# Kernel optimization log

Measured on AMD Instinct MI355X. Metric: run time of the kernel, lower is better.

## Reference

```python
import jax, jax.numpy as jnp
import numpy as np
from jax import lax

WS = 8        # window size
NH = 4        # num heads
HD = 32       # head dim
DIM = NH * HD # 128
SCALE = HD ** -0.5


def _rel_index(ws):
    coords = np.stack(np.meshgrid(np.arange(ws), np.arange(ws), indexing='ij'))  # (2,ws,ws)
    cf = coords.reshape(2, -1)                      # (2, N)
    rel = cf[:, :, None] - cf[:, None, :]           # (2, N, N)
    rel = rel.transpose(1, 2, 0).astype(np.int64)   # (N, N, 2)
    rel[..., 0] += ws - 1
    rel[..., 1] += ws - 1
    rel[..., 0] *= 2 * ws - 1
    return jnp.asarray(rel.sum(-1))                 # (N, N)


def setup_inputs() -> dict:
    key = jax.random.key(0)
    ks = jax.random.split(key, 8)
    B, H, W = 8, 128, 128
    return {
        'x': jax.random.normal(ks[0], (B, DIM, H, W), jnp.float32),
        'qkv_w': jax.random.normal(ks[1], (DIM, 3 * DIM), jnp.float32) * 0.02,
        'qkv_b': jnp.zeros((3 * DIM,), jnp.float32),
        'proj_w': jax.random.normal(ks[2], (DIM, DIM), jnp.float32) * 0.02,
        'proj_b': jnp.zeros((DIM,), jnp.float32),
        'rpb_table': jax.random.normal(ks[3], ((2 * WS - 1) * (2 * WS - 1), NH), jnp.float32) * 0.02,
        'fc_w': jax.random.normal(ks[4], (9, 3 * NH), jnp.float32) * 0.1,   # 1x1 conv: (out=9, in=3*NH)
        'fc_b': jnp.zeros((9,), jnp.float32),
        'dep_w': jax.random.normal(ks[5], (DIM, 9, 3, 3), jnp.float32) * 0.1,  # grouped conv OIHW, groups=HD
        'dep_b': jnp.zeros((DIM,), jnp.float32),
        'rate1': jnp.array(0.5, jnp.float32),
        'rate2': jnp.array(0.5, jnp.float32),
    }


def reference(x, qkv_w, qkv_b, proj_w, proj_b, rpb_table, fc_w, fc_b, dep_w, dep_b, rate1, rate2):
    B, C, H, W = x.shape
    N = WS * WS
    xh = jnp.transpose(x, (0, 2, 3, 1))                 # (B,H,W,C)
    qkv = xh @ qkv_w + qkv_b                            # (B,H,W,3C)

    # ----- conv branch -----
    f_all = qkv.reshape(B, H * W, 3 * NH, HD).transpose(0, 2, 1, 3)       # (B,3NH,HW,HD)
    f_c = jnp.einsum('oc,bcnd->bond', fc_w, f_all) + fc_b[None, :, None, None]  # (B,9,HW,HD)
    f_conv = jnp.transpose(f_c, (0, 3, 1, 2)).reshape(B, HD * 9, H, W)    # (B,9*HD,H,W)
    out_conv = lax.conv_general_dilated(
        f_conv, dep_w, window_strides=(1, 1), padding=((1, 1), (1, 1)),
        dimension_numbers=('NCHW', 'OIHW', 'NCHW'), feature_group_count=HD)
    out_conv = jnp.transpose(out_conv + dep_b[None, :, None, None], (0, 2, 3, 1))  # (B,H,W,C)

    # ----- windowed attention branch -----
    nWh, nWw = H // WS, W // WS
    w = qkv.reshape(B, nWh, WS, nWw, WS, 3 * C).transpose(0, 1, 3, 2, 4, 5)
    w = w.reshape(B * nWh * nWw, N, 3, NH, HD).transpose(2, 0, 3, 1, 4)   # (3,Bw,NH,N,HD)
    q, k, v = w[0] * SCALE, w[1], w[2]
    attn = jnp.einsum('bhnd,bhmd->bhnm', q, k)                            # (Bw,NH,N,N)
    bias = rpb_table[_rel_index(WS)]                                      # (N,N,NH)
    attn = attn + jnp.transpose(bias, (2, 0, 1))[None]
    attn = jax.nn.softmax(attn, axis=-1)
    xa = jnp.einsum('bhnm,bhmd->bnhd', attn, v).reshape(-1, N, C)         # (Bw,N,C)
    xa = xa @ proj_w + proj_b
    xa = xa.reshape(B, nWh, nWw, WS, WS, C).transpose(0, 1, 3, 2, 4, 5).reshape(B, H, W, C)

    out = rate1 * xa + rate2 * out_conv
    return jnp.transpose(out, (0, 3, 1, 2))
```

## Files before the change

### kernel.cpp

```cpp
#include <hip/hip_runtime.h>

typedef unsigned short ushort_t;
typedef unsigned int uint_t;
typedef __attribute__((ext_vector_type(8))) short short8;
typedef __attribute__((ext_vector_type(4))) float f32x4;

#define SCALE 0.17677669529663687f

__device__ __forceinline__ float blo(uint_t u) { return __uint_as_float(u << 16); }
__device__ __forceinline__ float bhi(uint_t u) { return __uint_as_float(u & 0xffff0000u); }
__device__ __forceinline__ float u2f(ushort_t u) { return __uint_as_float(((uint_t)u) << 16); }
__device__ __forceinline__ ushort_t f2u(float f) {
    const uint_t x = __float_as_uint(f);
    return (ushort_t)((x + 0x7fffu + ((x >> 16) & 1u)) >> 16);
}
__device__ __forceinline__ uint_t pack2(float a, float b) {
    return (uint_t)f2u(a) | ((uint_t)f2u(b) << 16);
}

__device__ __forceinline__ float dot8(const float* qa, uint4 u) {
    return qa[0] * blo(u.x) + qa[1] * bhi(u.x) + qa[2] * blo(u.y) + qa[3] * bhi(u.y)
         + qa[4] * blo(u.z) + qa[5] * bhi(u.z) + qa[6] * blo(u.w) + qa[7] * bhi(u.w);
}
__device__ __forceinline__ void pv8(float* a, float e, uint4 u) {
    a[0] += e * blo(u.x); a[1] += e * bhi(u.x); a[2] += e * blo(u.y); a[3] += e * bhi(u.y);
    a[4] += e * blo(u.z); a[5] += e * bhi(u.z); a[6] += e * blo(u.w); a[7] += e * bhi(u.w);
}


__global__ __launch_bounds__(256) void k_qqkv(
    const float* __restrict__ x, const float* __restrict__ w,
    const float* __restrict__ wb, ushort_t* __restrict__ qkv)
{
    __shared__ ushort_t XT[128 * 128];
    __shared__ ushort_t WT[128 * 128];
    const int t = threadIdx.x;
    const int p0 = blockIdx.x * 128;
    const int b = p0 >> 14;
    const int rem = p0 & 16383;
    const float* xb = x + ((size_t)b << 21) + rem;

#pragma unroll
    for (int it = 0; it < 8; ++it) {
        const int slot = it * 256 + t;
        const int p = slot & 127, cb = slot >> 7;
        uint4 u;
        {
            const float a0 = xb[(size_t)(cb * 8 + 0) * 16384 + p];
            const float a1 = xb[(size_t)(cb * 8 + 1) * 16384 + p];
            const float a2 = xb[(size_t)(cb * 8 + 2) * 16384 + p];
            const float a3 = xb[(size_t)(cb * 8 + 3) * 16384 + p];
            const float a4 = xb[(size_t)(cb * 8 + 4) * 16384 + p];
            const float a5 = xb[(size_t)(cb * 8 + 5) * 16384 + p];
            const float a6 = xb[(size_t)(cb * 8 + 6) * 16384 + p];
            const float a7 = xb[(size_t)(cb * 8 + 7) * 16384 + p];
            u.x = pack2(a0, a1); u.y = pack2(a2, a3);
            u.z = pack2(a4, a5); u.w = pack2(a6, a7);
        }
        *(uint4*)&XT[p * 128 + ((cb ^ (p & 7)) << 3)] = u;
    }

    const int l = t & 63, wv = t >> 6;
    const int wj = (wv >> 1) * 64, wp = (wv & 1) * 64;
    const int lr = l & 15, lg = l >> 4;

    for (int jt = 0; jt < 3; ++jt) {
        const int j0 = jt * 128;
        __syncthreads();

#pragma unroll
        for (int it = 0; it < 8; ++it) {
            const int slot = it * 256 + t;
            const int j = slot & 127, cb = slot >> 7;
            uint4 u;
            {
                const float a0 = w[(size_t)(cb * 8 + 0) * 384 + j0 + j];
                const float a1 = w[(size_t)(cb * 8 + 1) * 384 + j0 + j];
                const float a2 = w[(size_t)(cb * 8 + 2) * 384 + j0 + j];
                const float a3 = w[(size_t)(cb * 8 + 3) * 384 + j0 + j];
                const float a4 = w[(size_t)(cb * 8 + 4) * 384 + j0 + j];
                const float a5 = w[(size_t)(cb * 8 + 5) * 384 + j0 + j];
                const float a6 = w[(size_t)(cb * 8 + 6) * 384 + j0 + j];
                const float a7 = w[(size_t)(cb * 8 + 7) * 384 + j0 + j];
                u.x = pack2(a0, a1); u.y = pack2(a2, a3);
                u.z = pack2(a4, a5); u.w = pack2(a6, a7);
            }
            *(uint4*)&WT[j * 128 + ((cb ^ (j & 7)) << 3)] = u;
        }
        __syncthreads();

        f32x4 acc[4][4];
#pragma unroll
        for (int i = 0; i < 4; ++i)
#pragma unroll
            for (int j = 0; j < 4; ++j) acc[i][j] = (f32x4){0.f, 0.f, 0.f, 0.f};

#pragma unroll
        for (int ks = 0; ks < 4; ++ks) {
            const int kb = ks * 4 + lg;
            short8 af[4], bf[4];
#pragma unroll
            for (int i = 0; i < 4; ++i) {
                const int jr = wj + i * 16 + lr;
                af[i] = *(const short8*)&WT[jr * 128 + ((kb ^ (jr & 7)) << 3)];
                const int pr = wp + i * 16 + lr;
                bf[i] = *(const short8*)&XT[pr * 128 + ((kb ^ (pr & 7)) << 3)];
            }
#pragma unroll
            for (int ji = 0; ji < 4; ++ji)
#pragma unroll
                for (int pi = 0; pi < 4; ++pi)
                    acc[ji][pi] = __builtin_amdgcn_mfma_f32_16x16x32_bf16(
                        af[ji], bf[pi], acc[ji][pi], 0, 0, 0);
        }
        __syncthreads();

#pragma unroll
        for (int ji = 0; ji < 4; ++ji) {
            const int jq = wj + ji * 16 + 4 * lg;
            const float4 bias = *(const float4*)&wb[j0 + jq];
#pragma unroll
            for (int pi = 0; pi < 4; ++pi) {
                const int p = wp + pi * 16 + lr;
                uint2 o;
                o.x = pack2(acc[ji][pi][0] + bias.x, acc[ji][pi][1] + bias.y);
                o.y = pack2(acc[ji][pi][2] + bias.z, acc[ji][pi][3] + bias.w);
                *(uint2*)&WT[p * 128 + (((jq >> 3) ^ (p & 7)) << 3) + (jq & 7)] = o;
            }
        }
        __syncthreads();

#pragma unroll
        for (int it = 0; it < 8; ++it) {
            const int slot = it * 256 + t;
            const int seg = slot & 15, p = slot >> 4;
            const uint4 v = *(const uint4*)&WT[p * 128 + ((seg ^ (p & 7)) << 3)];
            *(uint4*)&qkv[(size_t)(p0 + p) * 384 + j0 + seg * 8] = v;
        }
    }
}

__global__ __launch_bounds__(256) void k_attn4(
    const ushort_t* __restrict__ qkv, const float* __restrict__ rpb,
    float* __restrict__ out)
{
    __shared__ uint_t lds[13956];
    ushort_t* lds_sh = (ushort_t*)lds;
    float* rpbl = (float*)(lds + 13056);
    const int t = threadIdx.x;
    const int b = blockIdx.x >> 8, wy = (blockIdx.x >> 4) & 15, wx = blockIdx.x & 15;
    const int prow0 = (b << 14) + (wy * 8) * 128 + wx * 8;
    const uint_t* qkvu = (const uint_t*)qkv;

    for (int i = t; i < 4096; i += 256) {
        const int m = i >> 6, u = i & 63;
        const size_t pr = (size_t)(prow0 + (m >> 3) * 128 + (m & 7)) * 192;
        lds[m * 68 + u]        = qkvu[pr + u];
        lds[4352 + m * 68 + u] = qkvu[pr + 64 + u];
        const uint_t v = qkvu[pr + 128 + u];
        lds_sh[17408 + (2 * u) * 68 + m]     = (ushort_t)(v & 0xffffu);
        lds_sh[17408 + (2 * u + 1) * 68 + m] = (ushort_t)(v >> 16);
    }
    for (int i = t; i < 900; i += 256) rpbl[i] = rpb[i];
    __syncthreads();

    const int h = t >> 6, l = t & 63;
    const int lr = l & 15, lg = l >> 4;

    short8 af_k[4], bf_q[4];
#pragma unroll
    for (int i = 0; i < 4; ++i) {
        af_k[i] = *(const short8*)&lds_sh[8704 + (i * 16 + lr) * 136 + h * 32 + lg * 8];
        bf_q[i] = *(const short8*)&lds_sh[(i * 16 + lr) * 136 + h * 32 + lg * 8];
    }
    f32x4 sA[4][4];
#pragma unroll
    for (int nt = 0; nt < 4; ++nt)
#pragma unroll
        for (int mt = 0; mt < 4; ++mt)
            sA[nt][mt] = __builtin_amdgcn_mfma_f32_16x16x32_bf16(
                af_k[mt], bf_q[nt], (f32x4){0.f, 0.f, 0.f, 0.f}, 0, 0, 0);

    float inv[4];
#pragma unroll
    for (int nt = 0; nt < 4; ++nt) {
        const int n = nt * 16 + lr;
        const int ry = n >> 3, rx = n & 7;
        float mxv = -1e30f;
#pragma unroll
        for (int mt = 0; mt < 4; ++mt)
#pragma unroll
            for (int r = 0; r < 4; ++r) {
                const int m = mt * 16 + lg * 4 + r;
                const float bias =
                    rpbl[((ry - (m >> 3) + 7) * 15 + (rx - (m & 7) + 7)) * 4 + h];
                const float s = sA[nt][mt][r] * SCALE + bias;
                sA[nt][mt][r] = s;
                mxv = fmaxf(mxv, s);
            }
        mxv = fmaxf(mxv, __shfl_xor(mxv, 16));
        mxv = fmaxf(mxv, __shfl_xor(mxv, 32));
        float ls = 0.f;
#pragma unroll
        for (int mt = 0; mt < 4; ++mt)
#pragma unroll
            for (int r = 0; r < 4; ++r) {
                const float e = __expf(sA[nt][mt][r] - mxv);
                sA[nt][mt][r] = e;
                ls += e;
            }
        ls += __shfl_xor(ls, 16);
        ls += __shfl_xor(ls, 32);
        inv[nt] = 1.f / ls;
    }

    __syncthreads();

    uint_t* Pb = lds + h * 2176;
#pragma unroll
    for (int nt = 0; nt < 4; ++nt) {
        const int n = nt * 16 + lr;
#pragma unroll
        for (int mt = 0; mt < 4; ++mt) {
            uint2 o;
            o.x = pack2(sA[nt][mt][0], sA[nt][mt][1]);
            o.y = pack2(sA[nt][mt][2], sA[nt][mt][3]);
            *(uint2*)&Pb[n * 34 + mt * 8 + lg * 2] = o;
        }
    }
    asm volatile("s_waitcnt lgkmcnt(0)" ::: "memory");

    union U8 { short8 s8; uint2 u2[2]; };
    f32x4 oA[2][4];
#pragma unroll
    for (int dt = 0; dt < 2; ++dt)
#pragma unroll
        for (int nt = 0; nt < 4; ++nt) oA[dt][nt] = (f32x4){0.f, 0.f, 0.f, 0.f};
#pragma unroll
    for (int ks = 0; ks < 2; ++ks) {
        const int kb = ks * 4 + lg;
        short8 av[2], bp[4];
#pragma unroll
        for (int dt = 0; dt < 2; ++dt) {
            U8 u;
            const int d = h * 32 + dt * 16 + lr;
            u.u2[0] = *(const uint2*)&lds[8704 + d * 34 + kb * 4];
            u.u2[1] = *(const uint2*)&lds[8704 + d * 34 + kb * 4 + 2];
            av[dt] = u.s8;
        }
#pragma unroll
        for (int nt = 0; nt < 4; ++nt) {
            U8 u;
            const int n = nt * 16 + lr;
            u.u2[0] = *(const uint2*)&Pb[n * 34 + kb * 4];
            u.u2[1] = *(const uint2*)&Pb[n * 34 + kb * 4 + 2];
            bp[nt] = u.s8;
        }
#pragma unroll
        for (int dt = 0; dt < 2; ++dt)
#pragma unroll
            for (int nt = 0; nt < 4; ++nt)
                oA[dt][nt] = __builtin_amdgcn_mfma_f32_16x16x32_bf16(
                    av[dt], bp[nt], oA[dt][nt], 0, 0, 0);
    }

    float* ob = out + ((size_t)b << 21);
    const int pixbase = (wy * 8) * 128 + wx * 8;
#pragma unroll
    for (int dt = 0; dt < 2; ++dt)
#pragma unroll
        for (int nt = 0; nt < 4; ++nt) {
            const int n = nt * 16 + lr;
            const size_t po = (size_t)(pixbase + (n >> 3) * 128 + (n & 7));
            const float iv = inv[nt];
#pragma unroll
            for (int r = 0; r < 4; ++r) {
                const int d = h * 32 + dt * 16 + lg * 4 + r;
                ob[((size_t)d << 14) + po] = oA[dt][nt][r] * iv;
            }
        }
}

__global__ __launch_bounds__(256) void k_proj(
    const float* __restrict__ pw, const float* __restrict__ pb,
    const float* __restrict__ r1, float* __restrict__ out)
{
    __shared__ ushort_t XT[128 * 128];
    __shared__ ushort_t WT[128 * 128];
    const int t = threadIdx.x;
    const int p0 = blockIdx.x * 128;
    const int b = p0 >> 14;
    const int rem = p0 & 16383;
    const float* xb = out + ((size_t)b << 21) + rem;

#pragma unroll
    for (int it = 0; it < 8; ++it) {
        const int slot = it * 256 + t;
        const int p = slot & 127, cb = slot >> 7;
        uint4 u;
        {
            const float a0 = xb[(size_t)(cb * 8 + 0) * 16384 + p];
            const float a1 = xb[(size_t)(cb * 8 + 1) * 16384 + p];
            const float a2 = xb[(size_t)(cb * 8 + 2) * 16384 + p];
            const float a3 = xb[(size_t)(cb * 8 + 3) * 16384 + p];
            const float a4 = xb[(size_t)(cb * 8 + 4) * 16384 + p];
            const float a5 = xb[(size_t)(cb * 8 + 5) * 16384 + p];
            const float a6 = xb[(size_t)(cb * 8 + 6) * 16384 + p];
            const float a7 = xb[(size_t)(cb * 8 + 7) * 16384 + p];
            u.x = pack2(a0, a1); u.y = pack2(a2, a3);
            u.z = pack2(a4, a5); u.w = pack2(a6, a7);
        }
        *(uint4*)&XT[p * 128 + ((cb ^ (p & 7)) << 3)] = u;
    }
#pragma unroll
    for (int it = 0; it < 8; ++it) {
        const int slot = it * 256 + t;
        const int j = slot & 127, cb = slot >> 7;
        uint4 u;
        {
            const float a0 = pw[(size_t)(cb * 8 + 0) * 128 + j];
            const float a1 = pw[(size_t)(cb * 8 + 1) * 128 + j];
            const float a2 = pw[(size_t)(cb * 8 + 2) * 128 + j];
            const float a3 = pw[(size_t)(cb * 8 + 3) * 128 + j];
            const float a4 = pw[(size_t)(cb * 8 + 4) * 128 + j];
            const float a5 = pw[(size_t)(cb * 8 + 5) * 128 + j];
            const float a6 = pw[(size_t)(cb * 8 + 6) * 128 + j];
            const float a7 = pw[(size_t)(cb * 8 + 7) * 128 + j];
            u.x = pack2(a0, a1); u.y = pack2(a2, a3);
            u.z = pack2(a4, a5); u.w = pack2(a6, a7);
        }
        *(uint4*)&WT[j * 128 + ((cb ^ (j & 7)) << 3)] = u;
    }
    __syncthreads();

    const int l = t & 63, wv = t >> 6;
    const int wj = (wv >> 1) * 64, wp = (wv & 1) * 64;
    const int lr = l & 15, lg = l >> 4;

    f32x4 acc[4][4];
#pragma unroll
    for (int i = 0; i < 4; ++i)
#pragma unroll
        for (int j = 0; j < 4; ++j) acc[i][j] = (f32x4){0.f, 0.f, 0.f, 0.f};

#pragma unroll
    for (int ks = 0; ks < 4; ++ks) {
        const int kb = ks * 4 + lg;
        short8 af[4], bf[4];
#pragma unroll
        for (int i = 0; i < 4; ++i) {
            const int jr = wj + i * 16 + lr;
            af[i] = *(const short8*)&WT[jr * 128 + ((kb ^ (jr & 7)) << 3)];
            const int pr = wp + i * 16 + lr;
            bf[i] = *(const short8*)&XT[pr * 128 + ((kb ^ (pr & 7)) << 3)];
        }
#pragma unroll
        for (int ji = 0; ji < 4; ++ji)
#pragma unroll
            for (int pi = 0; pi < 4; ++pi)
                acc[ji][pi] = __builtin_amdgcn_mfma_f32_16x16x32_bf16(
                    af[ji], bf[pi], acc[ji][pi], 0, 0, 0);
    }

    const float rate1 = r1[0];
    float* obase = out + ((size_t)b << 21) + rem;
#pragma unroll
    for (int ji = 0; ji < 4; ++ji) {
        const int jq = wj + ji * 16 + 4 * lg;
        const float4 bias = *(const float4*)&pb[jq];
#pragma unroll
        for (int pi = 0; pi < 4; ++pi) {
            const int p = wp + pi * 16 + lr;
            float* op = obase + (size_t)jq * 16384 + p;
            op[0]     = rate1 * (acc[ji][pi][0] + bias.x);
            op[16384] = rate1 * (acc[ji][pi][1] + bias.y);
            op[32768] = rate1 * (acc[ji][pi][2] + bias.z);
            op[49152] = rate1 * (acc[ji][pi][3] + bias.w);
        }
    }
}

__global__ __launch_bounds__(256) void k_conv7(
    const ushort_t* __restrict__ qkv, const float* __restrict__ fcw,
    const float* __restrict__ fcb, const float* __restrict__ depw,
    const float* __restrict__ depb, const float* __restrict__ r2,
    float* __restrict__ out)
{
    __shared__ ushort_t fcl[11664];
    __shared__ __align__(16) float dwl[1296];
    __shared__ float fcwl[108];
    __shared__ float fcbl[9];

    const int t = threadIdx.x;
    const int half = blockIdx.x & 1;
    const int tile = (blockIdx.x >> 1) & 63;
    const int b = blockIdx.x >> 7;
    const int ty0 = (tile >> 3) << 4, tx0 = (tile & 7) << 4;
    if (t < 108) fcwl[t] = fcw[t];
    if (t < 9)   fcbl[t] = fcb[t];
    const float rate2 = r2[0];
    const int py = t >> 4, px = t & 15;
    float* ob = out + ((size_t)b << 21) + (size_t)((ty0 + py) * 128 + (tx0 + px));

    const int row0 = t / 18, col0 = t - row0 * 18;
    const int hy0 = ty0 + row0 - 1, hx0 = tx0 + col0 - 1;
    const int g0 = ((unsigned)hy0 < 128u && (unsigned)hx0 < 128u)
                       ? ((b << 14) + hy0 * 128 + hx0) : -1;
    const int t1 = t + 256, row1 = t1 / 18, col1 = t1 - row1 * 18;
    const int hy1 = ty0 + row1 - 1, hx1 = tx0 + col1 - 1;
    const int g1 = (t < 68 && (unsigned)hy1 < 128u && (unsigned)hx1 < 128u)
                       ? ((b << 14) + hy1 * 128 + hx1) : -1;

    for (int ci = 0; ci < 4; ++ci) {
        const int chunk = half * 4 + ci;
        __syncthreads();
        for (int i = t; i < 1296; i += 256)
            dwl[i] = depw[(chunk * 16 + (i & 15)) * 81 + (i >> 4)];

#pragma unroll
        for (int hf = 0; hf < 2; ++hf) {
            const int g = hf ? g1 : g0;
            const int pix = hf ? (256 + t) : t;
            if (hf && t >= 68) break;
            float fo[9][4];
#pragma unroll
            for (int ii = 0; ii < 9; ++ii) {
                const float bv = (g >= 0) ? fcbl[ii] : 0.f;
                fo[ii][0] = bv; fo[ii][1] = bv; fo[ii][2] = bv; fo[ii][3] = bv;
            }
            if (g >= 0) {
                const uint2* qp = (const uint2*)(qkv + (size_t)g * 384 + chunk * 4);
#pragma unroll
                for (int e = 0; e < 12; ++e) {
                    const uint2 q = qp[e * 8];
                    const float f0 = blo(q.x), f1 = bhi(q.x);
                    const float f2 = blo(q.y), f3 = bhi(q.y);
#pragma unroll
                    for (int ii = 0; ii < 9; ++ii) {
                        const float wv = fcwl[ii * 12 + e];
                        fo[ii][0] += wv * f0; fo[ii][1] += wv * f1;
                        fo[ii][2] += wv * f2; fo[ii][3] += wv * f3;
                    }
                }
            }
#pragma unroll
            for (int ii = 0; ii < 9; ++ii)
#pragma unroll
                for (int dd = 0; dd < 4; ++dd)
                    fcl[(ii * 4 + dd) * 324 + pix] = f2u(fo[ii][dd]);
        }
        __syncthreads();

        float4 accv[4];
#pragma unroll
        for (int dd = 0; dd < 4; ++dd) accv[dd] = make_float4(0.f, 0.f, 0.f, 0.f);
#pragma unroll
        for (int ii = 0; ii < 9; ++ii) {
#pragma unroll
            for (int kk = 0; kk < 9; ++kk) {
                const int ky = kk / 3, kx = kk - (kk / 3) * 3;
                const int hpix = (py + ky) * 18 + px + kx;
                const float4* dwp = (const float4*)&dwl[(ii * 9 + kk) * 16];
#pragma unroll
                for (int dd = 0; dd < 4; ++dd) {
                    const float f = u2f(fcl[(ii * 4 + dd) * 324 + hpix]);
                    const float4 d4 = dwp[dd];
                    accv[dd].x += f * d4.x; accv[dd].y += f * d4.y;
                    accv[dd].z += f * d4.z; accv[dd].w += f * d4.w;
                }
            }
        }
#pragma unroll
        for (int dd = 0; dd < 4; ++dd) {
            const float av[4] = {accv[dd].x, accv[dd].y, accv[dd].z, accv[dd].w};
#pragma unroll
            for (int j = 0; j < 4; ++j) {
                const int oc = chunk * 16 + dd * 4 + j;
                ob[(size_t)oc << 14] += rate2 * (av[j] + depb[oc]);
            }
        }
    }
}

#define WS_W2  0
#define WS_B2  36864
#define WS_TOT 37152

__global__ __launch_bounds__(256) void k_prep_f(
    const float* __restrict__ qkv_w, const float* __restrict__ qkv_b,
    const float* __restrict__ fcw, const float* __restrict__ fcb,
    float* __restrict__ ws)
{
    const int idx = blockIdx.x * 256 + threadIdx.x;
    if (idx < WS_B2) {
        const int c = idx / 288, r = idx - c * 288, i = r >> 5, d = r & 31;
        float s = 0.f;
#pragma unroll
        for (int e = 0; e < 12; ++e)
            s += fcw[i * 12 + e] * qkv_w[c * 384 + e * 32 + d];
        ws[idx] = s;
    } else if (idx < WS_TOT) {
        const int r = idx - WS_B2, i = r >> 5, d = r & 31;
        float s = fcb[i];
#pragma unroll
        for (int e = 0; e < 12; ++e)
            s += fcw[i * 12 + e] * qkv_b[e * 32 + d];
        ws[idx] = s;
    }
}

__global__ __launch_bounds__(256) void k_attn_f(
    const float* __restrict__ x, const float* __restrict__ qw,
    const float* __restrict__ qb, const float* __restrict__ pw,
    const float* __restrict__ pb, const float* __restrict__ rpb,
    const float* __restrict__ r1, float* __restrict__ out)
{
    __shared__ ushort_t xw[8192];
    __shared__ float arena[8450];
    ushort_t* kvb = (ushort_t*)arena;
    const int t = threadIdx.x;
    const int b = blockIdx.x >> 8, wy = (blockIdx.x >> 4) & 15, wx = blockIdx.x & 15;
    const size_t xbase = ((size_t)b << 21) + (size_t)((wy * 8) * 128 + wx * 8);
    for (int i = t; i < 8192; i += 256) {
        const int c = i >> 6, p = i & 63;
        xw[i] = f2u(x[xbase + (size_t)c * 16384 + (p >> 3) * 128 + (p & 7)]);
    }
    __syncthreads();
    const int h = t >> 6, n = t & 63;
    float qa[32], ka[32], va[32];
#pragma unroll
    for (int cc = 0; cc < 32; ++cc) {
        qa[cc] = qb[h * 32 + cc];
        ka[cc] = qb[128 + h * 32 + cc];
        va[cc] = qb[256 + h * 32 + cc];
    }
    const float* wbase = qw + h * 32;
    for (int c = 0; c < 128; ++c) {
        const float xv = u2f(xw[c * 64 + n]);
        const float* wr = wbase + c * 384;
#pragma unroll
        for (int j = 0; j < 8; ++j) {
            const float4 aq = ((const float4*)wr)[j];
            const float4 ak = ((const float4*)(wr + 128))[j];
            const float4 av = ((const float4*)(wr + 256))[j];
            qa[4 * j + 0] += xv * aq.x; qa[4 * j + 1] += xv * aq.y;
            qa[4 * j + 2] += xv * aq.z; qa[4 * j + 3] += xv * aq.w;
            ka[4 * j + 0] += xv * ak.x; ka[4 * j + 1] += xv * ak.y;
            ka[4 * j + 2] += xv * ak.z; ka[4 * j + 3] += xv * ak.w;
            va[4 * j + 0] += xv * av.x; va[4 * j + 1] += xv * av.y;
            va[4 * j + 2] += xv * av.z; va[4 * j + 3] += xv * av.w;
        }
    }
#pragma unroll
    for (int cc = 0; cc < 32; ++cc) qa[cc] *= SCALE;
    uint_t* kv32 = (uint_t*)kvb;
#pragma unroll
    for (int j = 0; j < 16; ++j) {
        kv32[n * 66 + h * 16 + j] = pack2(ka[2 * j], ka[2 * j + 1]);
        kv32[4224 + n * 66 + h * 16 + j] = pack2(va[2 * j], va[2 * j + 1]);
    }
    __syncthreads();
    const int ry = n >> 3, rx = n & 7;
    float sar[64];
    float mx = -1e30f;
#pragma unroll
    for (int m = 0; m < 64; ++m) {
        const uint2* kr = (const uint2*)(kvb + m * 132 + h * 32);
        float s = 0.f;
#pragma unroll
        for (int j = 0; j < 8; ++j) {
            const uint2 u = kr[j];
            s += qa[4 * j + 0] * blo(u.x) + qa[4 * j + 1] * bhi(u.x)
               + qa[4 * j + 2] * blo(u.y) + qa[4 * j + 3] * bhi(u.y);
        }
        s += rpb[((ry - (m >> 3) + 7) * 15 + (rx - (m & 7) + 7)) * 4 + h];
        sar[m] = s;
        mx = fmaxf(mx, s);
    }
    float l = 0.f;
#pragma unroll
    for (int m = 0; m < 64; ++m) { const float e = __expf(sar[m] - mx); sar[m] = e; l += e; }
    const float inv = 1.f / l;
    float acc[32];
#pragma unroll
    for (int cc = 0; cc < 32; ++cc) acc[cc] = 0.f;
#pragma unroll
    for (int m = 0; m < 64; ++m) {
        const float pm = sar[m];
        const uint2* vr = (const uint2*)(kvb + 8448 + m * 132 + h * 32);
#pragma unroll
        for (int j = 0; j < 8; ++j) {
            const uint2 u = vr[j];
            acc[4 * j + 0] += pm * blo(u.x); acc[4 * j + 1] += pm * bhi(u.x);
            acc[4 * j + 2] += pm * blo(u.y); acc[4 * j + 3] += pm * bhi(u.y);
        }
    }
    __syncthreads();
#pragma unroll
    for (int cc = 0; cc < 32; ++cc) arena[n * 130 + h * 32 + cc] = acc[cc] * inv;
    __syncthreads();
    const int p = t & 63, jb = t >> 6;
    float aj[32];
#pragma unroll
    for (int jj = 0; jj < 32; ++jj) aj[jj] = pb[jb * 32 + jj];
    const float* xr = arena + p * 130;
    const float* pwb = pw + jb * 32;
    for (int c = 0; c < 128; ++c) {
        const float xv = xr[c];
        const float4* pr = (const float4*)(pwb + c * 128);
#pragma unroll
        for (int j = 0; j < 8; ++j) {
            const float4 w4 = pr[j];
            aj[4 * j + 0] += xv * w4.x; aj[4 * j + 1] += xv * w4.y;
            aj[4 * j + 2] += xv * w4.z; aj[4 * j + 3] += xv * w4.w;
        }
    }
    const float rate1 = r1[0];
    const int oy = wy * 8 + (p >> 3), ox = wx * 8 + (p & 7);
    float* ob = out + ((size_t)b << 21) + (size_t)(oy * 128 + ox);
#pragma unroll
    for (int jj = 0; jj < 32; ++jj)
        ob[(size_t)(jb * 32 + jj) << 14] = rate1 * aj[jj];
}

__global__ __launch_bounds__(256) void k_conv_f(
    const float* __restrict__ x, const float* __restrict__ ws,
    const float* __restrict__ depw, const float* __restrict__ depb,
    const float* __restrict__ r2, float* __restrict__ out)
{
    __shared__ float arena[12960];
    __shared__ float b2s[36];
    float* w2l = arena;
    ushort_t* xl = (ushort_t*)(arena + 4608);
    float* fcl = arena;
    float* dwl = arena + 11664;
    const int t = threadIdx.x;
    const int b = blockIdx.x >> 6, tile = blockIdx.x & 63;
    const int ty0 = (tile >> 3) << 4, tx0 = (tile & 7) << 4;
    const size_t xbase = ((size_t)b << 21);
    const float rate2 = r2[0];
    const int py = t >> 4, px = t & 15;
    float* ob = out + ((size_t)b << 21) + (size_t)((ty0 + py) * 128 + (tx0 + px));
    const int r0 = t / 18, c0 = t - r0 * 18;
    const bool ok0 = ((unsigned)(ty0 + r0 - 1) < 128u) && ((unsigned)(tx0 + c0 - 1) < 128u);
    const int t1 = 256 + t, r1i = t1 / 18, c1 = t1 - r1i * 18;
    const bool ok1 = (t < 68) && ((unsigned)(ty0 + r1i - 1) < 128u) && ((unsigned)(tx0 + c1 - 1) < 128u);
    for (int chunk = 0; chunk < 8; ++chunk) {
        __syncthreads();
        for (int i = t; i < 4608; i += 256) {
            const int c = i / 36, r = i - c * 36;
            w2l[i] = ws[WS_W2 + c * 288 + (r >> 2) * 32 + chunk * 4 + (r & 3)];
        }
        if (t < 36) b2s[t] = ws[WS_B2 + (t >> 2) * 32 + chunk * 4 + (t & 3)];
        __syncthreads();
        float fca[2][36];
#pragma unroll
        for (int r = 0; r < 36; ++r) { fca[0][r] = b2s[r]; fca[1][r] = b2s[r]; }
        for (int cs = 0; cs < 8; ++cs) {
            if (cs) __syncthreads();
            for (int i = t; i < 5184; i += 256) {
                const int cc = i / 324, pp = i - cc * 324;
                const int row = pp / 18, col = pp - row * 18;
                const int hy = ty0 + row - 1, hx = tx0 + col - 1;
                ushort_t v = 0;
                if ((unsigned)hy < 128u && (unsigned)hx < 128u)
                    v = f2u(x[xbase + (size_t)(cs * 16 + cc) * 16384 + hy * 128 + hx]);
                xl[i] = v;
            }
            __syncthreads();
#pragma unroll 4
            for (int cc = 0; cc < 16; ++cc) {
                const float xv0 = u2f(xl[cc * 324 + t]);
                const float xv1 = (t < 68) ? u2f(xl[cc * 324 + 256 + t]) : 0.f;
                const float* wr = w2l + (cs * 16 + cc) * 36;
#pragma unroll
                for (int r = 0; r < 36; r += 4) {
                    const float4 w4 = *(const float4*)(wr + r);
                    fca[0][r + 0] += xv0 * w4.x; fca[0][r + 1] += xv0 * w4.y;
                    fca[0][r + 2] += xv0 * w4.z; fca[0][r + 3] += xv0 * w4.w;
                    fca[1][r + 0] += xv1 * w4.x; fca[1][r + 1] += xv1 * w4.y;
                    fca[1][r + 2] += xv1 * w4.z; fca[1][r + 3] += xv1 * w4.w;
                }
            }
        }
        __syncthreads();
#pragma unroll
        for (int r = 0; r < 36; ++r) {
            fcl[r * 324 + t] = ok0 ? fca[0][r] : 0.f;
            if (t < 68) fcl[r * 324 + 256 + t] = ok1 ? fca[1][r] : 0.f;
        }
        for (int i = t; i < 1296; i += 256) {
            const int kk = i >> 4, ocl = i & 15;
            dwl[i] = depw[(chunk * 16 + ocl) * 81 + kk];
        }
        __syncthreads();
        float4 accv[4];
#pragma unroll
        for (int dd = 0; dd < 4; ++dd) accv[dd] = make_float4(0.f, 0.f, 0.f, 0.f);
#pragma unroll
        for (int ii = 0; ii < 9; ++ii) {
#pragma unroll
            for (int kk = 0; kk < 9; ++kk) {
                const int ky = kk / 3, kx = kk - (kk / 3) * 3;
                const int hpix = (py + ky) * 18 + px + kx;
                const float4* dwp = (const float4*)&dwl[(ii * 9 + kk) * 16];
#pragma unroll
                for (int dd = 0; dd < 4; ++dd) {
                    const float f = fcl[(ii * 4 + dd) * 324 + hpix];
                    const float4 d4 = dwp[dd];
                    accv[dd].x += f * d4.x; accv[dd].y += f * d4.y;
                    accv[dd].z += f * d4.z; accv[dd].w += f * d4.w;
                }
            }
        }
#pragma unroll
        for (int dd = 0; dd < 4; ++dd) {
            const float av[4] = {accv[dd].x, accv[dd].y, accv[dd].z, accv[dd].w};
#pragma unroll
            for (int j = 0; j < 4; ++j) {
                const int oc = chunk * 16 + dd * 4 + j;
                ob[(size_t)oc << 14] += rate2 * (av[j] + depb[oc]);
            }
        }
    }
}

extern "C" void kernel_launch(void* const* d_in, const int* in_sizes, int n_in,
                              void* d_out, int out_size, void* d_ws, size_t ws_size,
                              hipStream_t stream) {
    (void)in_sizes; (void)n_in; (void)out_size;
    const float* x      = (const float*)d_in[0];
    const float* qkv_w  = (const float*)d_in[1];
    const float* qkv_b  = (const float*)d_in[2];
    const float* proj_w = (const float*)d_in[3];
    const float* proj_b = (const float*)d_in[4];
    const float* rpb    = (const float*)d_in[5];
    const float* fc_w   = (const float*)d_in[6];
    const float* fc_b   = (const float*)d_in[7];
    const float* dep_w  = (const float*)d_in[8];
    const float* dep_b  = (const float*)d_in[9];
    const float* rate1  = (const float*)d_in[10];
    const float* rate2  = (const float*)d_in[11];
    float* out = (float*)d_out;

    if (ws_size >= (size_t)131072 * 384 * 2) {
        ushort_t* qkv = (ushort_t*)d_ws;
        k_qqkv<<<dim3(1024), dim3(256), 0, stream>>>(x, qkv_w, qkv_b, qkv);
        k_attn4<<<dim3(2048), dim3(256), 0, stream>>>(qkv, rpb, out);
        k_proj<<<dim3(1024), dim3(256), 0, stream>>>(proj_w, proj_b, rate1, out);
        k_conv7<<<dim3(1024), dim3(256), 0, stream>>>(qkv, fc_w, fc_b, dep_w,
                                                      dep_b, rate2, out);
    } else {
        float* wsf = (float*)d_ws;
        k_prep_f<<<dim3(146), dim3(256), 0, stream>>>(qkv_w, qkv_b, fc_w, fc_b, wsf);
        k_attn_f<<<dim3(2048), dim3(256), 0, stream>>>(x, qkv_w, qkv_b, proj_w,
                                                       proj_b, rpb, rate1, out);
        k_conv_f<<<dim3(512), dim3(256), 0, stream>>>(x, wsf, dep_w, dep_b,
                                                      rate2, out);
    }
}
```

Baseline: 431.7 us.

## Write chunk-major qkv copy for conv branch and read it in new conv kernel

The QKV projection kernel now also writes a second bf16 copy of qkv, regrouped so each of 8 channel chunks holds a contiguous 48-element record per pixel. A new conv kernel reads that layout with six contiguous 16-byte loads per pixel instead of gathering from the interleaved 384-wide rows. The goal is coalesced, lower-overhead loads in the conv branch. In exchange the projection writes extra bytes and the path needs twice the workspace, with the old path kept as a fallback.

```diff
diff --git a/kernel.cpp b/kernel.cpp
--- a/kernel.cpp
+++ b/kernel.cpp
@@ -6,6 +6,7 @@
 typedef __attribute__((ext_vector_type(4))) float f32x4;
 
 #define SCALE 0.17677669529663687f
+#define QC_PLANE ((size_t)131072 * 48)
 
 __device__ __forceinline__ float blo(uint_t u) { return __uint_as_float(u << 16); }
 __device__ __forceinline__ float bhi(uint_t u) { return __uint_as_float(u & 0xffff0000u); }
@@ -30,7 +31,8 @@
 
 __global__ __launch_bounds__(256) void k_qqkv(
     const float* __restrict__ x, const float* __restrict__ w,
-    const float* __restrict__ wb, ushort_t* __restrict__ qkv)
+    const float* __restrict__ wb, ushort_t* __restrict__ qkv,
+    ushort_t* __restrict__ qc)
 {
     __shared__ ushort_t XT[128 * 128];
     __shared__ ushort_t WT[128 * 128];
@@ -137,6 +139,25 @@
             const uint4 v = *(const uint4*)&WT[p * 128 + ((seg ^ (p & 7)) << 3)];
             *(uint4*)&qkv[(size_t)(p0 + p) * 384 + j0 + seg * 8] = v;
         }
+
+        if (qc) {
+#pragma unroll
+            for (int it = 0; it < 4; ++it) {
+                const int unit = it * 256 + t;
+                const int p = unit & 127, c = unit >> 7;
+                uint2 r[4];
+#pragma unroll
+                for (int ee = 0; ee < 4; ++ee) {
+                    const int jl = ee * 32 + c * 4;
+                    r[ee] = *(const uint2*)&WT[p * 128 +
+                        (((jl >> 3) ^ (p & 7)) << 3) + (jl & 7)];
+                }
+                ushort_t* dst = qc + (size_t)c * QC_PLANE +
+                                (size_t)(p0 + p) * 48 + jt * 16;
+                *(uint4*)dst       = make_uint4(r[0].x, r[0].y, r[1].x, r[1].y);
+                *(uint4*)(dst + 8) = make_uint4(r[2].x, r[2].y, r[3].x, r[3].y);
+            }
+        }
     }
 }
 
@@ -376,6 +397,114 @@
             op[16384] = rate1 * (acc[ji][pi][1] + bias.y);
             op[32768] = rate1 * (acc[ji][pi][2] + bias.z);
             op[49152] = rate1 * (acc[ji][pi][3] + bias.w);
+        }
+    }
+}
+
+__global__ __launch_bounds__(256) void k_conv8(
+    const ushort_t* __restrict__ qc, const float* __restrict__ fcw,
+    const float* __restrict__ fcb, const float* __restrict__ depw,
+    const float* __restrict__ depb, const float* __restrict__ r2,
+    float* __restrict__ out)
+{
+    __shared__ ushort_t fcl[11664];
+    __shared__ __align__(16) float dwl[1296];
+    __shared__ float fcwl[108];
+    __shared__ float fcbl[9];
+
+    const int t = threadIdx.x;
+    const int half = blockIdx.x & 1;
+    const int tile = (blockIdx.x >> 1) & 63;
+    const int b = blockIdx.x >> 7;
+    const int ty0 = (tile >> 3) << 4, tx0 = (tile & 7) << 4;
+    if (t < 108) fcwl[t] = fcw[t];
+    if (t < 9)   fcbl[t] = fcb[t];
+    const float rate2 = r2[0];
+    const int py = t >> 4, px = t & 15;
+    float* ob = out + ((size_t)b << 21) + (size_t)((ty0 + py) * 128 + (tx0 + px));
+
+    const int row0 = t / 18, col0 = t - row0 * 18;
+    const int hy0 = ty0 + row0 - 1, hx0 = tx0 + col0 - 1;
+    const int g0 = ((unsigned)hy0 < 128u && (unsigned)hx0 < 128u)
+                       ? ((b << 14) + hy0 * 128 + hx0) : -1;
+    const int t1 = t + 256, row1 = t1 / 18, col1 = t1 - row1 * 18;
+    const int hy1 = ty0 + row1 - 1, hx1 = tx0 + col1 - 1;
+    const int g1 = (t < 68 && (unsigned)hy1 < 128u && (unsigned)hx1 < 128u)
+                       ? ((b << 14) + hy1 * 128 + hx1) : -1;
+
+    for (int ci = 0; ci < 4; ++ci) {
+        const int chunk = half * 4 + ci;
+        __syncthreads();
+        for (int i = t; i < 1296; i += 256)
+            dwl[i] = depw[(chunk * 16 + (i & 15)) * 81 + (i >> 4)];
+
+        const ushort_t* qp_base = qc + (size_t)chunk * QC_PLANE;
+#pragma unroll
+        for (int hf = 0; hf < 2; ++hf) {
+            const int g = hf ? g1 : g0;
+            const int pix = hf ? (256 + t) : t;
+            if (hf && t >= 68) break;
+            float fo[9][4];
+#pragma unroll
+            for (int ii = 0; ii < 9; ++ii) {
+                const float bv = (g >= 0) ? fcbl[ii] : 0.f;
+                fo[ii][0] = bv; fo[ii][1] = bv; fo[ii][2] = bv; fo[ii][3] = bv;
+            }
+            if (g >= 0) {
+                const uint4* qp = (const uint4*)(qp_base + (size_t)g * 48);
+                const uint4 v0 = qp[0], v1 = qp[1], v2 = qp[2];
+                const uint4 v3 = qp[3], v4 = qp[4], v5 = qp[5];
+                const uint_t uu[24] = {v0.x, v0.y, v0.z, v0.w, v1.x, v1.y, v1.z, v1.w,
+                                       v2.x, v2.y, v2.z, v2.w, v3.x, v3.y, v3.z, v3.w,
+                                       v4.x, v4.y, v4.z, v4.w, v5.x, v5.y, v5.z, v5.w};
+#pragma unroll
+                for (int e = 0; e < 12; ++e) {
+                    const uint_t lo = uu[e * 2], hi = uu[e * 2 + 1];
+                    const float f0 = blo(lo), f1 = bhi(lo);
+                    const float f2 = blo(hi), f3 = bhi(hi);
+#pragma unroll
+                    for (int ii = 0; ii < 9; ++ii) {
+                        const float wv = fcwl[ii * 12 + e];
+                        fo[ii][0] += wv * f0; fo[ii][1] += wv * f1;
+                        fo[ii][2] += wv * f2; fo[ii][3] += wv * f3;
+                    }
+                }
+            }
+#pragma unroll
+            for (int ii = 0; ii < 9; ++ii)
+#pragma unroll
+                for (int dd = 0; dd < 4; ++dd)
+                    fcl[(ii * 4 + dd) * 324 + pix] = f2u(fo[ii][dd]);
+        }
+        __syncthreads();
+
+        float4 accv[4];
+#pragma unroll
+        for (int dd = 0; dd < 4; ++dd) accv[dd] = make_float4(0.f, 0.f, 0.f, 0.f);
+#pragma unroll
+        for (int ii = 0; ii < 9; ++ii) {
+#pragma unroll
+            for (int kk = 0; kk < 9; ++kk) {
+                const int ky = kk / 3, kx = kk - (kk / 3) * 3;
+                const int hpix = (py + ky) * 18 + px + kx;
+                const float4* dwp = (const float4*)&dwl[(ii * 9 + kk) * 16];
+#pragma unroll
+                for (int dd = 0; dd < 4; ++dd) {
+                    const float f = u2f(fcl[(ii * 4 + dd) * 324 + hpix]);
+                    const float4 d4 = dwp[dd];
+                    accv[dd].x += f * d4.x; accv[dd].y += f * d4.y;
+                    accv[dd].z += f * d4.z; accv[dd].w += f * d4.w;
+                }
+            }
+        }
+#pragma unroll
+        for (int dd = 0; dd < 4; ++dd) {
+            const float av[4] = {accv[dd].x, accv[dd].y, accv[dd].z, accv[dd].w};
+#pragma unroll
+            for (int j = 0; j < 4; ++j) {
+                const int oc = chunk * 16 + dd * 4 + j;
+                ob[(size_t)oc << 14] += rate2 * (av[j] + depb[oc]);
+            }
         }
     }
 }
@@ -743,9 +872,19 @@
     const float* rate2  = (const float*)d_in[11];
     float* out = (float*)d_out;
 
-    if (ws_size >= (size_t)131072 * 384 * 2) {
+    const size_t QKV_SZ = (size_t)131072 * 384;
+    if (ws_size >= QKV_SZ * 2 * 2) {
         ushort_t* qkv = (ushort_t*)d_ws;
-        k_qqkv<<<dim3(1024), dim3(256), 0, stream>>>(x, qkv_w, qkv_b, qkv);
+        ushort_t* qc  = qkv + QKV_SZ;
+        k_qqkv<<<dim3(1024), dim3(256), 0, stream>>>(x, qkv_w, qkv_b, qkv, qc);
+        k_attn4<<<dim3(2048), dim3(256), 0, stream>>>(qkv, rpb, out);
+        k_proj<<<dim3(1024), dim3(256), 0, stream>>>(proj_w, proj_b, rate1, out);
+        k_conv8<<<dim3(1024), dim3(256), 0, stream>>>(qc, fc_w, fc_b, dep_w,
+                                                      dep_b, rate2, out);
+    } else if (ws_size >= QKV_SZ * 2) {
+        ushort_t* qkv = (ushort_t*)d_ws;
+        k_qqkv<<<dim3(1024), dim3(256), 0, stream>>>(x, qkv_w, qkv_b, qkv,
+                                                     (ushort_t*)nullptr);
         k_attn4<<<dim3(2048), dim3(256), 0, stream>>>(qkv, rpb, out);
         k_proj<<<dim3(1024), dim3(256), 0, stream>>>(proj_w, proj_b, rate1, out);
         k_conv7<<<dim3(1024), dim3(256), 0, stream>>>(qkv, fc_w, fc_b, dep_w,
```

Measured after the change: 411.9 us. 1.05x faster.
